# Kernel optimization log

Measured on AMD Instinct MI355X. Metric: run time of the kernel, lower is better.

## Reference

```python
import jax, jax.numpy as jnp
import numpy as np

B, T, VOCAB_SZ, N_SPK = 64, 1024, 34, 128
D_TXT, D_SPK, H, N_MELS = 512, 64, 256, 80


def _lstm_params(key, in_dim, hid):
    k1, k2, k3, k4 = jax.random.split(key, 4)
    s = 1.0 / np.sqrt(hid)
    Wih = jax.random.uniform(k1, (4 * hid, in_dim), jnp.float32, -s, s)
    Whh = jax.random.uniform(k2, (4 * hid, hid), jnp.float32, -s, s)
    bih = jax.random.uniform(k3, (4 * hid,), jnp.float32, -s, s)
    bhh = jax.random.uniform(k4, (4 * hid,), jnp.float32, -s, s)
    return Wih, Whh, bih, bhh


def setup_inputs() -> dict:
    key = jax.random.key(0)
    ks = jax.random.split(key, 10)
    text_seq = jax.random.randint(ks[0], (B, T), 0, VOCAB_SZ)
    mel_spectrogram = jax.random.normal(ks[1], (B, T, N_MELS), jnp.float32)
    speaker_id = jax.random.randint(ks[2], (B,), 0, N_SPK)
    emb_text = jax.random.normal(ks[3], (VOCAB_SZ, D_TXT), jnp.float32)
    emb_text = emb_text.at[0].set(0.0)  # padding_idx=0
    emb_spk = jax.random.normal(ks[4], (N_SPK, D_SPK), jnp.float32)
    Wih_f, Whh_f, bih_f, bhh_f = _lstm_params(ks[5], D_TXT + D_SPK, H)
    Wih_b, Whh_b, bih_b, bhh_b = _lstm_params(ks[6], D_TXT + D_SPK, H)
    Wih_d, _Whh_d, bih_d, bhh_d = _lstm_params(ks[7], N_MELS + 2 * H, H)
    s = 1.0 / np.sqrt(H)
    Wfc = jax.random.uniform(ks[8], (N_MELS, H), jnp.float32, -s, s)
    bfc = jax.random.uniform(ks[9], (N_MELS,), jnp.float32, -s, s)
    return dict(text_seq=text_seq, mel_spectrogram=mel_spectrogram, speaker_id=speaker_id,
                emb_text=emb_text, emb_spk=emb_spk,
                Wih_f=Wih_f, Whh_f=Whh_f, bih_f=bih_f, bhh_f=bhh_f,
                Wih_b=Wih_b, Whh_b=Whh_b, bih_b=bih_b, bhh_b=bhh_b,
                Wih_d=Wih_d, bih_d=bih_d, bhh_d=bhh_d, Wfc=Wfc, bfc=bfc)


def _lstm_scan(xs, Wih, Whh, bih, bhh, reverse=False):
    # xs: [T, B, D] -> hs: [T, B, H] (PyTorch gate order i,f,g,o)
    nB, hid = xs.shape[1], Whh.shape[1]
    bias = bih + bhh
    def step(carry, x):
        h, c = carry
        g = x @ Wih.T + h @ Whh.T + bias
        i, f, gg, o = jnp.split(g, 4, axis=-1)
        c = jax.nn.sigmoid(f) * c + jax.nn.sigmoid(i) * jnp.tanh(gg)
        h = jax.nn.sigmoid(o) * jnp.tanh(c)
        return (h, c), h
    init = (jnp.zeros((nB, hid), xs.dtype), jnp.zeros((nB, hid), xs.dtype))
    _, hs = jax.lax.scan(step, init, xs, reverse=reverse)
    return hs


def reference(text_seq, mel_spectrogram, speaker_id, emb_text, emb_spk,
              Wih_f, Whh_f, bih_f, bhh_f, Wih_b, Whh_b, bih_b, bhh_b,
              Wih_d, bih_d, bhh_d, Wfc, bfc):
    text_embed = emb_text[text_seq]                       # [B, T, 512]
    spk = jnp.broadcast_to(emb_spk[speaker_id][:, None, :],
                           (text_seq.shape[0], text_seq.shape[1], emb_spk.shape[1]))
    enc_in = jnp.concatenate([text_embed, spk], axis=-1)  # [B, T, 576]
    xs = jnp.transpose(enc_in, (1, 0, 2))                 # time-major [T, B, 576]
    h_fwd = _lstm_scan(xs, Wih_f, Whh_f, bih_f, bhh_f)
    h_bwd = _lstm_scan(xs, Wih_b, Whh_b, bih_b, bhh_b, reverse=True)
    enc_out = jnp.concatenate([h_fwd, h_bwd], axis=-1)    # [T, B, 512]

    max_len = min(mel_spectrogram.shape[1], enc_out.shape[0])
    # Decoder: hidden state is reset (None) every step in the original, so
    # c = sigmoid(i)*tanh(g), h = sigmoid(o)*tanh(c); Whh contributes nothing.
    dbias = bih_d + bhh_d
    def dstep(prev_mel, e_t):
        x = jnp.concatenate([prev_mel, e_t], axis=-1)     # [B, 592]
        g = x @ Wih_d.T + dbias
        i, f, gg, o = jnp.split(g, 4, axis=-1)
        c = jax.nn.sigmoid(i) * jnp.tanh(gg)
        h = jax.nn.sigmoid(o) * jnp.tanh(c)
        out = h @ Wfc.T + bfc
        return out, out
    _, outs = jax.lax.scan(dstep, mel_spectrogram[:, 0, :], enc_out[: max_len - 1])
    return jnp.transpose(outs, (1, 0, 2))                 # [B, max_len-1, 80]
```

## Files before the change

kernel.cpp:

```cpp
#include <hip/hip_runtime.h>
#include <hip/hip_fp16.h>
#include <stdint.h>

#define T_SEQ 1024
#define NB    64
#define VOCAB 34
#define NSPK  128
#define DTXT  512
#define HID   256
#define NMEL  80
#define GROWS 1024
#define DROWS 768

typedef _Float16 f16;
typedef _Float16 f16x2 __attribute__((ext_vector_type(2)));
typedef _Float16 v8h __attribute__((ext_vector_type(8)));
typedef float v4f __attribute__((ext_vector_type(4)));

__device__ __forceinline__ float fdot2f(uint32_t a, uint32_t b, float c) {
  return __builtin_amdgcn_fdot2(__builtin_bit_cast(f16x2, a),
                                __builtin_bit_cast(f16x2, b), c, false);
}
__device__ __forceinline__ float sigm(float x) { return 1.0f / (1.0f + __expf(-x)); }
__device__ __forceinline__ float tanhf_fast(float x) {
  float e = __expf(2.0f * x);
  return 1.0f - 2.0f / (e + 1.0f);
}
__device__ __forceinline__ void bar_vperm() {
  asm volatile("s_waitcnt lgkmcnt(0)\n\ts_barrier" ::: "memory");
  __builtin_amdgcn_sched_barrier(0);
}


__global__ void k_tp(const float* __restrict__ Wf, const float* __restrict__ Wb,
                     const float* __restrict__ emb_text, float* __restrict__ TP) {
  int blk = blockIdx.x; int dir = blk / VOCAB; int v = blk - dir * VOCAB;
  const float* W = dir ? Wb : Wf;
  const float4* e4 = (const float4*)(emb_text + (size_t)v * DTXT);
  for (int r = threadIdx.x; r < GROWS; r += 256) {
    const float4* w4 = (const float4*)(W + (size_t)r * 576);
    float a0 = 0, a1 = 0, a2 = 0, a3 = 0;
    #pragma unroll 4
    for (int d = 0; d < DTXT / 4; ++d) {
      float4 ev = e4[d], wv = w4[d];
      a0 += ev.x * wv.x; a1 += ev.y * wv.y;
      a2 += ev.z * wv.z; a3 += ev.w * wv.w;
    }
    TP[(size_t)(dir * VOCAB + v) * GROWS + r] = (a0 + a1) + (a2 + a3);
  }
}

__global__ void k_sp(const float* __restrict__ Wf, const float* __restrict__ Wb,
                     const float* __restrict__ bihf, const float* __restrict__ bhhf,
                     const float* __restrict__ bihb, const float* __restrict__ bhhb,
                     const float* __restrict__ emb_spk, float* __restrict__ SP) {
  int blk = blockIdx.x; int dir = blk >> 7; int s = blk & 127;
  const float* W  = dir ? Wb : Wf;
  const float* bi = dir ? bihb : bihf;
  const float* bh = dir ? bhhb : bhhf;
  const float4* e4 = (const float4*)(emb_spk + (size_t)s * 64);
  for (int r = threadIdx.x; r < GROWS; r += 256) {
    const float4* w4 = (const float4*)(W + (size_t)r * 576 + 512);
    float a0 = 0, a1 = 0, a2 = 0, a3 = 0;
    #pragma unroll
    for (int d = 0; d < 16; ++d) {
      float4 ev = e4[d], wv = w4[d];
      a0 += ev.x * wv.x; a1 += ev.y * wv.y;
      a2 += ev.z * wv.z; a3 += ev.w * wv.w;
    }
    SP[(size_t)(dir * NSPK + s) * GROWS + r] = bi[r] + bh[r] + (a0 + a1) + (a2 + a3);
  }
}

__global__ void k_whh(const float* __restrict__ Whhf, const float* __restrict__ Whhb,
                      f16* __restrict__ WhhH) {
  int idx = blockIdx.x * 256 + threadIdx.x;
  if (idx < 2 * GROWS * HID) {
    int dir = idx >> 18; int rem = idx & (GROWS * HID - 1);
    WhhH[idx] = (f16)(dir ? Whhb[rem] : Whhf[rem]);
  }
}

__global__ void k_decw(const float* __restrict__ Wih_d, const float* __restrict__ bih_d,
                       const float* __restrict__ bhh_d,
                       f16* __restrict__ WmH, f16* __restrict__ WdH, float* __restrict__ dbias) {
  int r = blockIdx.x;
  int src = (r < 256) ? r : (r + 256);
  const float* w = Wih_d + (size_t)src * 592;
  for (int k = threadIdx.x; k < 592; k += 256) {
    float v = w[k];
    if (k < 80) WmH[(size_t)r * 80 + k] = (f16)v;
    else        WdH[(size_t)r * 512 + (k - 80)] = (f16)v;
  }
  if (threadIdx.x == 0) dbias[r] = bih_d[src] + bhh_d[src];
}

__global__ void k_misc(const float* __restrict__ Wfc, f16* __restrict__ WfcH) {
  int idx = blockIdx.x * 256 + threadIdx.x;
  if (idx < NMEL * HID) WfcH[idx] = (f16)Wfc[idx];
}

__launch_bounds__(512, 2)
__global__ void k_enc(const int* __restrict__ text_seq, const int* __restrict__ speaker_id,
                      const float* __restrict__ TP, const float* __restrict__ SP,
                      const uint32_t* __restrict__ WhhH_dw,
                      f16* __restrict__ Hh) {
  __shared__ __align__(16) uint4 wtail[16 * 512];
  __shared__ __align__(16) uint32_t hbuf[2][128];
  __shared__ float pp[4][256];
  __shared__ int tseq[T_SEQ];

  int wg = blockIdx.x;
  int dir = wg >> 6, b = wg & 63;
  int tid = threadIdx.x;
  int u = tid & 255, kh = tid >> 8;

  uint4 w0[12], w1[12], w2[12], w3[12];
  {
    const uint4* p0 = (const uint4*)(WhhH_dw + ((size_t)(dir << 10) + u      ) * 128 + (kh << 6));
    const uint4* p1 = (const uint4*)(WhhH_dw + ((size_t)(dir << 10) + u + 256) * 128 + (kh << 6));
    const uint4* p2 = (const uint4*)(WhhH_dw + ((size_t)(dir << 10) + u + 512) * 128 + (kh << 6));
    const uint4* p3 = (const uint4*)(WhhH_dw + ((size_t)(dir << 10) + u + 768) * 128 + (kh << 6));
    #pragma unroll
    for (int i = 0; i < 12; ++i) { w0[i] = p0[i]; w1[i] = p1[i]; w2[i] = p2[i]; w3[i] = p3[i]; }
    #pragma unroll
    for (int j = 0; j < 4; ++j) {
      wtail[(0 * 4 + j) * 512 + tid] = p0[12 + j];
      wtail[(1 * 4 + j) * 512 + tid] = p1[12 + j];
      wtail[(2 * 4 + j) * 512 + tid] = p2[12 + j];
      wtail[(3 * 4 + j) * 512 + tid] = p3[12 + j];
    }
  }
  for (int i = tid; i < T_SEQ; i += 512) tseq[i] = text_seq[b * T_SEQ + i];
  if (tid < 128) hbuf[0][tid] = 0u;
  float sp0 = 0, sp1 = 0, sp2 = 0, sp3 = 0;
  if (kh == 0) {
    int spk = speaker_id[b];
    sp0 = SP[(size_t)(dir * NSPK + spk) * GROWS + u];
    sp1 = SP[(size_t)(dir * NSPK + spk) * GROWS + u + 256];
    sp2 = SP[(size_t)(dir * NSPK + spk) * GROWS + u + 512];
    sp3 = SP[(size_t)(dir * NSPK + spk) * GROWS + u + 768];
  }
  const float* TPd = TP + (size_t)dir * VOCAB * GROWS;
  float c_state = 0.0f;
  __syncthreads();

  float x0 = 0, x1 = 0, x2 = 0, x3 = 0;
  if (kh == 0) {
    int v = tseq[dir ? (T_SEQ - 1) : 0];
    x0 = TPd[(size_t)v * GROWS + u];
    x1 = TPd[(size_t)v * GROWS + u + 256];
    x2 = TPd[(size_t)v * GROWS + u + 512];
    x3 = TPd[(size_t)v * GROWS + u + 768];
  }

  float h_keep = 0.0f; int t_keep = 0;
  for (int n = 0; n < T_SEQ; ++n) {
    int t = dir ? (T_SEQ - 1 - n) : n;
    float xn0 = 0, xn1 = 0, xn2 = 0, xn3 = 0;
    if (kh == 0) {
      if (n > 0)
        Hh[((size_t)(dir * T_SEQ + t_keep) * NB + b) * HID + u] = (f16)h_keep;
      int tn = dir ? (T_SEQ - 2 - n) : (n + 1);
      tn = tn < 0 ? 0 : (tn > T_SEQ - 1 ? T_SEQ - 1 : tn);
      int vn = tseq[tn];
      xn0 = TPd[(size_t)vn * GROWS + u];
      xn1 = TPd[(size_t)vn * GROWS + u + 256];
      xn2 = TPd[(size_t)vn * GROWS + u + 512];
      xn3 = TPd[(size_t)vn * GROWS + u + 768];
    }

    float i0 = 0, i1 = 0, f0 = 0, f1 = 0, g0 = 0, g1 = 0, o0 = 0, o1 = 0;
    const uint4* h4 = ((const uint4*)hbuf[n & 1]) + (kh << 4);
    #pragma unroll
    for (int c = 0; c < 12; ++c) {
      uint4 hv = h4[c];
      i0 = fdot2f(w0[c].x, hv.x, i0); f0 = fdot2f(w1[c].x, hv.x, f0);
      g0 = fdot2f(w2[c].x, hv.x, g0); o0 = fdot2f(w3[c].x, hv.x, o0);
      i1 = fdot2f(w0[c].y, hv.y, i1); f1 = fdot2f(w1[c].y, hv.y, f1);
      g1 = fdot2f(w2[c].y, hv.y, g1); o1 = fdot2f(w3[c].y, hv.y, o1);
      i0 = fdot2f(w0[c].z, hv.z, i0); f0 = fdot2f(w1[c].z, hv.z, f0);
      g0 = fdot2f(w2[c].z, hv.z, g0); o0 = fdot2f(w3[c].z, hv.z, o0);
      i1 = fdot2f(w0[c].w, hv.w, i1); f1 = fdot2f(w1[c].w, hv.w, f1);
      g1 = fdot2f(w2[c].w, hv.w, g1); o1 = fdot2f(w3[c].w, hv.w, o1);
    }
    #pragma unroll
    for (int j = 0; j < 4; ++j) {
      uint4 hv = h4[12 + j];
      uint4 t0v = wtail[(0 * 4 + j) * 512 + tid];
      uint4 t1v = wtail[(1 * 4 + j) * 512 + tid];
      uint4 t2v = wtail[(2 * 4 + j) * 512 + tid];
      uint4 t3v = wtail[(3 * 4 + j) * 512 + tid];
      i0 = fdot2f(t0v.x, hv.x, i0); f0 = fdot2f(t1v.x, hv.x, f0);
      g0 = fdot2f(t2v.x, hv.x, g0); o0 = fdot2f(t3v.x, hv.x, o0);
      i1 = fdot2f(t0v.y, hv.y, i1); f1 = fdot2f(t1v.y, hv.y, f1);
      g1 = fdot2f(t2v.y, hv.y, g1); o1 = fdot2f(t3v.y, hv.y, o1);
      i0 = fdot2f(t0v.z, hv.z, i0); f0 = fdot2f(t1v.z, hv.z, f0);
      g0 = fdot2f(t2v.z, hv.z, g0); o0 = fdot2f(t3v.z, hv.z, o0);
      i1 = fdot2f(t0v.w, hv.w, i1); f1 = fdot2f(t1v.w, hv.w, f1);
      g1 = fdot2f(t2v.w, hv.w, g1); o1 = fdot2f(t3v.w, hv.w, o1);
    }
    if (kh == 1) {
      pp[0][u] = i0 + i1;
      pp[1][u] = f0 + f1;
      pp[2][u] = g0 + g1;
      pp[3][u] = o0 + o1;
    }
    bar_vperm();

    if (kh == 0) {
      float gi = (i0 + i1) + pp[0][u] + x0 + sp0;
      float gf = (f0 + f1) + pp[1][u] + x1 + sp1;
      float gg = (g0 + g1) + pp[2][u] + x2 + sp2;
      float go = (o0 + o1) + pp[3][u] + x3 + sp3;
      c_state = sigm(gf) * c_state + sigm(gi) * tanhf_fast(gg);
      float h = sigm(go) * tanhf_fast(c_state);
      ((f16*)hbuf[(n + 1) & 1])[u] = (f16)h;
      h_keep = h; t_keep = t;
      x0 = xn0; x1 = xn1; x2 = xn2; x3 = xn3;
    }
    bar_vperm();
  }
  if (kh == 0)
    Hh[((size_t)(dir * T_SEQ + t_keep) * NB + b) * HID + u] = (f16)h_keep;
}

__launch_bounds__(256, 4)
__global__ void k_eproj(const uint32_t* __restrict__ Hdw, const uint32_t* __restrict__ WdH_dw,
                        const float* __restrict__ dbias, f16* __restrict__ E) {
  __shared__ __align__(16) uint32_t Asm[64][68];
  __shared__ __align__(16) uint32_t Wsm[64][68];
  int nt = blockIdx.x % 12;
  int t  = blockIdx.x / 12;
  int n0 = nt * 64;
  int tid = threadIdx.x;
  int wave = tid >> 6, lane = tid & 63;
  int lr = lane & 15, lg = lane >> 4;

  v4f acc0 = {0,0,0,0}, acc1 = {0,0,0,0}, acc2 = {0,0,0,0}, acc3 = {0,0,0,0};

  for (int ch = 0; ch < 4; ++ch) {
    int dirc = ch >> 1, koff = (ch & 1) * 64;
    {
      int bb = tid >> 2, p = tid & 3;
      const uint32_t* asrc = Hdw + ((size_t)(dirc * T_SEQ + t) * NB + bb) * 128 + koff + p * 4;
      const uint32_t* wsrc = WdH_dw + (size_t)(n0 + bb) * 256 + ch * 64 + p * 4;
      #pragma unroll
      for (int q = 0; q < 4; ++q) {
        *(uint4*)(&Asm[bb][p * 4 + q * 16]) = *(const uint4*)(asrc + q * 16);
        *(uint4*)(&Wsm[bb][p * 4 + q * 16]) = *(const uint4*)(wsrc + q * 16);
      }
    }
    __syncthreads();
    #pragma unroll
    for (int sub = 0; sub < 4; ++sub) {
      v8h af = __builtin_bit_cast(v8h, *(const uint4*)&Asm[wave * 16 + lr][sub * 16 + lg * 4]);
      v8h b0 = __builtin_bit_cast(v8h, *(const uint4*)&Wsm[ 0 + lr][sub * 16 + lg * 4]);
      v8h b1 = __builtin_bit_cast(v8h, *(const uint4*)&Wsm[16 + lr][sub * 16 + lg * 4]);
      v8h b2 = __builtin_bit_cast(v8h, *(const uint4*)&Wsm[32 + lr][sub * 16 + lg * 4]);
      v8h b3 = __builtin_bit_cast(v8h, *(const uint4*)&Wsm[48 + lr][sub * 16 + lg * 4]);
      acc0 = __builtin_amdgcn_mfma_f32_16x16x32_f16(af, b0, acc0, 0, 0, 0);
      acc1 = __builtin_amdgcn_mfma_f32_16x16x32_f16(af, b1, acc1, 0, 0, 0);
      acc2 = __builtin_amdgcn_mfma_f32_16x16x32_f16(af, b2, acc2, 0, 0, 0);
      acc3 = __builtin_amdgcn_mfma_f32_16x16x32_f16(af, b3, acc3, 0, 0, 0);
    }
    __syncthreads();
  }

  float db0 = dbias[n0 +  0 + lr];
  float db1 = dbias[n0 + 16 + lr];
  float db2 = dbias[n0 + 32 + lr];
  float db3 = dbias[n0 + 48 + lr];
  #pragma unroll
  for (int reg = 0; reg < 4; ++reg) {
    int m = wave * 16 + lg * 4 + reg;
    f16* Erow = E + ((size_t)t * NB + m) * DROWS + n0;
    Erow[ 0 + lr] = (f16)(acc0[reg] + db0);
    Erow[16 + lr] = (f16)(acc1[reg] + db1);
    Erow[32 + lr] = (f16)(acc2[reg] + db2);
    Erow[48 + lr] = (f16)(acc3[reg] + db3);
  }
}

__launch_bounds__(512, 2)
__global__ void k_dec(const float* __restrict__ mel, const f16* __restrict__ E,
                      const uint32_t* __restrict__ WmH_dw, const uint32_t* __restrict__ WfcH_dw,
                      const float* __restrict__ bfc, float* __restrict__ out) {
  __shared__ __align__(16) uint32_t pm[40];
  __shared__ __align__(16) uint32_t h_sm[128];
  __shared__ float pp[3][256];
  __shared__ float partial[80][4];
  __shared__ __align__(16) uint4 Ebuf[2][16 * 96];

  int b = blockIdx.x;
  int tid = threadIdx.x;
  int u = tid & 255, kh = tid >> 8;

  uint4 wm0[5], wm1[5], wm2[5];
  {
    const uint4* p0 = (const uint4*)(WmH_dw + (size_t)(u      ) * 40) + kh * 5;
    const uint4* p1 = (const uint4*)(WmH_dw + (size_t)(u + 256) * 40) + kh * 5;
    const uint4* p2 = (const uint4*)(WmH_dw + (size_t)(u + 512) * 40) + kh * 5;
    #pragma unroll
    for (int k = 0; k < 5; ++k) { wm0[k] = p0[k]; wm1[k] = p1[k]; wm2[k] = p2[k]; }
  }
  int fr = (tid < 320) ? (tid >> 2) : 0;
  int q  = tid & 3;
  uint4 wfc[8];
  {
    const uint4* wp = (const uint4*)(WfcH_dw + (size_t)fr * 128) + q * 8;
    #pragma unroll
    for (int k = 0; k < 8; ++k) wfc[k] = wp[k];
  }
  float bfcv = bfc[tid < NMEL ? tid : 0];
  if (tid < 40) {
    float m0 = mel[(size_t)b * T_SEQ * NMEL + 2 * tid];
    float m1 = mel[(size_t)b * T_SEQ * NMEL + 2 * tid + 1];
    f16x2 v; v[0] = (f16)m0; v[1] = (f16)m1;
    pm[tid] = __builtin_bit_cast(uint32_t, v);
  }

  int srow = tid >> 5, scol = tid & 31;
  {
    const uint4* src = (const uint4*)(E + ((size_t)srow * NB + b) * DROWS);
    Ebuf[0][srow * 96 + scol     ] = src[scol];
    Ebuf[0][srow * 96 + scol + 32] = src[scol + 32];
    Ebuf[0][srow * 96 + scol + 64] = src[scol + 64];
  }
  __syncthreads();

  float o_keep = 0.0f;
  for (int t = 0; t < T_SEQ - 1; ++t) {
    int w = t >> 4, s = t & 15;
    if (t > 0 && tid < NMEL)
      out[((size_t)b * (T_SEQ - 1) + (t - 1)) * NMEL + tid] = o_keep;
    uint4 st0, st1, st2;
    bool do_stage = (s == 0) && (w < 63);
    if (do_stage) {
      int rr = (w + 1) * 16 + srow; if (rr > T_SEQ - 2) rr = T_SEQ - 2;
      const uint4* src = (const uint4*)(E + ((size_t)rr * NB + b) * DROWS);
      st0 = src[scol]; st1 = src[scol + 32]; st2 = src[scol + 64];
    }

    float a0 = 0, a1 = 0, a2 = 0;
    const uint4* pm4 = ((const uint4*)pm) + kh * 5;
    #pragma unroll
    for (int k = 0; k < 5; ++k) {
      uint4 hp = pm4[k];
      a0 = fdot2f(wm0[k].x, hp.x, a0); a1 = fdot2f(wm1[k].x, hp.x, a1); a2 = fdot2f(wm2[k].x, hp.x, a2);
      a0 = fdot2f(wm0[k].y, hp.y, a0); a1 = fdot2f(wm1[k].y, hp.y, a1); a2 = fdot2f(wm2[k].y, hp.y, a2);
      a0 = fdot2f(wm0[k].z, hp.z, a0); a1 = fdot2f(wm1[k].z, hp.z, a1); a2 = fdot2f(wm2[k].z, hp.z, a2);
      a0 = fdot2f(wm0[k].w, hp.w, a0); a1 = fdot2f(wm1[k].w, hp.w, a1); a2 = fdot2f(wm2[k].w, hp.w, a2);
    }
    if (kh == 1) { pp[0][u] = a0; pp[1][u] = a1; pp[2][u] = a2; }
    __syncthreads();

    if (kh == 0) {
      const f16* Erow = (const f16*)&Ebuf[w & 1][s * 96];
      float gi = a0 + pp[0][u] + (float)Erow[u];
      float gg = a1 + pp[1][u] + (float)Erow[u + 256];
      float go = a2 + pp[2][u] + (float)Erow[u + 512];
      float cc = sigm(gi) * tanhf_fast(gg);
      float h  = sigm(go) * tanhf_fast(cc);
      ((f16*)h_sm)[u] = (f16)h;
    }
    if (do_stage) {
      Ebuf[(w + 1) & 1][srow * 96 + scol     ] = st0;
      Ebuf[(w + 1) & 1][srow * 96 + scol + 32] = st1;
      Ebuf[(w + 1) & 1][srow * 96 + scol + 64] = st2;
    }
    __syncthreads();

    if (tid < 320) {
      const uint4* hrow = ((const uint4*)h_sm) + q * 8;
      float s0 = 0, s1 = 0, s2 = 0, s3 = 0;
      #pragma unroll
      for (int kk = 0; kk < 8; ++kk) {
        uint4 hq = hrow[kk];
        s0 = fdot2f(wfc[kk].x, hq.x, s0); s1 = fdot2f(wfc[kk].y, hq.y, s1);
        s2 = fdot2f(wfc[kk].z, hq.z, s2); s3 = fdot2f(wfc[kk].w, hq.w, s3);
      }
      partial[fr][q] = (s0 + s1) + (s2 + s3);
    }
    __syncthreads();

    if (tid < NMEL) {
      float o = ((partial[tid][0] + partial[tid][1]) +
                 (partial[tid][2] + partial[tid][3])) + bfcv;
      o_keep = o;
      ((f16*)pm)[tid] = (f16)o;
    }
    __syncthreads();
  }
  if (tid < NMEL)
    out[((size_t)b * (T_SEQ - 1) + (T_SEQ - 2)) * NMEL + tid] = o_keep;
}

extern "C" void kernel_launch(void* const* d_in, const int* in_sizes, int n_in,
                              void* d_out, int out_size, void* d_ws, size_t ws_size,
                              hipStream_t stream) {
  const int*   text_seq   = (const int*)d_in[0];
  const float* mel        = (const float*)d_in[1];
  const int*   speaker_id = (const int*)d_in[2];
  const float* emb_text   = (const float*)d_in[3];
  const float* emb_spk    = (const float*)d_in[4];
  const float* Wih_f = (const float*)d_in[5];
  const float* Whh_f = (const float*)d_in[6];
  const float* bih_f = (const float*)d_in[7];
  const float* bhh_f = (const float*)d_in[8];
  const float* Wih_b = (const float*)d_in[9];
  const float* Whh_b = (const float*)d_in[10];
  const float* bih_b = (const float*)d_in[11];
  const float* bhh_b = (const float*)d_in[12];
  const float* Wih_d = (const float*)d_in[13];
  const float* bih_d = (const float*)d_in[14];
  const float* bhh_d = (const float*)d_in[15];
  const float* Wfc   = (const float*)d_in[16];
  const float* bfc   = (const float*)d_in[17];
  float* out = (float*)d_out;

  char* base = (char*)d_ws;
  size_t off = 0;
  auto take = [&](size_t n) -> char* {
    off = (off + 255) & ~(size_t)255;
    char* r = base + off;
    off += n;
    return r;
  };
  float*        TP    = (float*)take((size_t)2 * VOCAB * GROWS * 4);
  float*        SP    = (float*)take((size_t)2 * NSPK * GROWS * 4);
  f16*          WhhH  = (f16*)take((size_t)2 * GROWS * HID * 2);
  f16*          WmH   = (f16*)take((size_t)DROWS * 80 * 2);
  f16*          WdH   = (f16*)take((size_t)DROWS * 512 * 2);
  f16*          WfcH  = (f16*)take((size_t)NMEL * HID * 2);
  float*        dbias = (float*)take((size_t)DROWS * 4);
  f16*          Hh    = (f16*)take((size_t)2 * T_SEQ * NB * HID * 2);
  f16*          E     = (f16*)take((size_t)(T_SEQ - 1) * NB * DROWS * 2);
  if (off > ws_size) return;

  k_tp  <<<2 * VOCAB, 256, 0, stream>>>(Wih_f, Wih_b, emb_text, TP);
  k_sp  <<<2 * NSPK, 256, 0, stream>>>(Wih_f, Wih_b, bih_f, bhh_f, bih_b, bhh_b, emb_spk, SP);
  k_whh <<<2048, 256, 0, stream>>>(Whh_f, Whh_b, WhhH);
  k_decw<<<DROWS, 256, 0, stream>>>(Wih_d, bih_d, bhh_d, WmH, WdH, dbias);
  k_misc<<<80, 256, 0, stream>>>(Wfc, WfcH);
  k_enc <<<128, 512, 0, stream>>>(text_seq, speaker_id, TP, SP,
                                  (const uint32_t*)WhhH, Hh);
  k_eproj<<<(T_SEQ - 1) * 12, 256, 0, stream>>>((const uint32_t*)Hh,
                                                (const uint32_t*)WdH, dbias, E);
  k_dec <<<NB, 512, 0, stream>>>(mel, E, (const uint32_t*)WmH,
                                 (const uint32_t*)WfcH, bfc, out);
}
```

Baseline: 2.834 ms.

## Split each encoder LSTM sequence across two workgroups with flag-based hidden-state exchange

The encoder recurrence now runs on two workgroups per (direction, batch) pair instead of one. Each workgroup owns half of the hidden units, keeps its full Whh rows in registers (dropping the LDS weight tail and the intra-block k-split reduction), and exchanges its half of h with its partner every step through global memory, using release/acquire flags that k_misc zeroes beforehand. This halves the per-step dot-product work and register/LDS pressure per workgroup and uses more CUs. In exchange it adds a cross-workgroup global-memory handshake on the serial critical path every timestep, and it deadlocks if the two partner workgroups are not co-resident. A large dummy LDS allocation is added, apparently to limit occupancy to one block per CU.

```diff
diff --git a/kernel.cpp b/kernel.cpp
--- a/kernel.cpp
+++ b/kernel.cpp
@@ -95,134 +95,102 @@
   if (threadIdx.x == 0) dbias[r] = bih_d[src] + bhh_d[src];
 }
 
-__global__ void k_misc(const float* __restrict__ Wfc, f16* __restrict__ WfcH) {
+__global__ void k_misc(const float* __restrict__ Wfc, f16* __restrict__ WfcH,
+                       unsigned int* __restrict__ flags) {
   int idx = blockIdx.x * 256 + threadIdx.x;
   if (idx < NMEL * HID) WfcH[idx] = (f16)Wfc[idx];
+  if (blockIdx.x == 0) flags[threadIdx.x * 64] = 0u;
 }
 
 __launch_bounds__(512, 2)
 __global__ void k_enc(const int* __restrict__ text_seq, const int* __restrict__ speaker_id,
                       const float* __restrict__ TP, const float* __restrict__ SP,
                       const uint32_t* __restrict__ WhhH_dw,
-                      f16* __restrict__ Hh) {
-  __shared__ __align__(16) uint4 wtail[16 * 512];
-  __shared__ __align__(16) uint32_t hbuf[2][128];
-  __shared__ float pp[4][256];
+                      f16* __restrict__ Hh, uint32_t* __restrict__ Hx,
+                      unsigned int* __restrict__ flags) {
+  __shared__ __align__(16) uint32_t hfull[2][128];
+  __shared__ float pp[512];
   __shared__ int tseq[T_SEQ];
-
-  int wg = blockIdx.x;
-  int dir = wg >> 6, b = wg & 63;
+  __shared__ __align__(16) uint4 lds_pad[4800];
+
+  int wgid = blockIdx.x;
+  int pair = wgid & 127, half = wgid >> 7;
+  int dir = pair >> 6, b = pair & 63;
   int tid = threadIdx.x;
-  int u = tid & 255, kh = tid >> 8;
-
-  uint4 w0[12], w1[12], w2[12], w3[12];
+  int g = tid >> 7, uu = tid & 127;
+  int row = g * 256 + half * 128 + uu;
+
+  uint4 w[32];
   {
-    const uint4* p0 = (const uint4*)(WhhH_dw + ((size_t)(dir << 10) + u      ) * 128 + (kh << 6));
-    const uint4* p1 = (const uint4*)(WhhH_dw + ((size_t)(dir << 10) + u + 256) * 128 + (kh << 6));
-    const uint4* p2 = (const uint4*)(WhhH_dw + ((size_t)(dir << 10) + u + 512) * 128 + (kh << 6));
-    const uint4* p3 = (const uint4*)(WhhH_dw + ((size_t)(dir << 10) + u + 768) * 128 + (kh << 6));
-    #pragma unroll
-    for (int i = 0; i < 12; ++i) { w0[i] = p0[i]; w1[i] = p1[i]; w2[i] = p2[i]; w3[i] = p3[i]; }
-    #pragma unroll
-    for (int j = 0; j < 4; ++j) {
-      wtail[(0 * 4 + j) * 512 + tid] = p0[12 + j];
-      wtail[(1 * 4 + j) * 512 + tid] = p1[12 + j];
-      wtail[(2 * 4 + j) * 512 + tid] = p2[12 + j];
-      wtail[(3 * 4 + j) * 512 + tid] = p3[12 + j];
-    }
+    const uint4* wp = (const uint4*)(WhhH_dw + ((size_t)(dir << 10) + row) * 128);
+    #pragma unroll
+    for (int i = 0; i < 32; ++i) w[i] = wp[i];
   }
   for (int i = tid; i < T_SEQ; i += 512) tseq[i] = text_seq[b * T_SEQ + i];
-  if (tid < 128) hbuf[0][tid] = 0u;
-  float sp0 = 0, sp1 = 0, sp2 = 0, sp3 = 0;
-  if (kh == 0) {
-    int spk = speaker_id[b];
-    sp0 = SP[(size_t)(dir * NSPK + spk) * GROWS + u];
-    sp1 = SP[(size_t)(dir * NSPK + spk) * GROWS + u + 256];
-    sp2 = SP[(size_t)(dir * NSPK + spk) * GROWS + u + 512];
-    sp3 = SP[(size_t)(dir * NSPK + spk) * GROWS + u + 768];
-  }
+  if (tid < 128) hfull[0][tid] = 0u;
+  ((volatile uint32_t*)lds_pad)[tid] = 0u;
+  float sp = SP[(size_t)(dir * NSPK + speaker_id[b]) * GROWS + row];
   const float* TPd = TP + (size_t)dir * VOCAB * GROWS;
   float c_state = 0.0f;
+  const unsigned myF = (unsigned)(pair * 2 + half);
+  const unsigned paF = (unsigned)(pair * 2 + (half ^ 1));
   __syncthreads();
 
-  float x0 = 0, x1 = 0, x2 = 0, x3 = 0;
-  if (kh == 0) {
-    int v = tseq[dir ? (T_SEQ - 1) : 0];
-    x0 = TPd[(size_t)v * GROWS + u];
-    x1 = TPd[(size_t)v * GROWS + u + 256];
-    x2 = TPd[(size_t)v * GROWS + u + 512];
-    x3 = TPd[(size_t)v * GROWS + u + 768];
-  }
-
-  float h_keep = 0.0f; int t_keep = 0;
+  float xcur = TPd[(size_t)tseq[dir ? (T_SEQ - 1) : 0] * GROWS + row];
+
   for (int n = 0; n < T_SEQ; ++n) {
     int t = dir ? (T_SEQ - 1 - n) : n;
-    float xn0 = 0, xn1 = 0, xn2 = 0, xn3 = 0;
-    if (kh == 0) {
-      if (n > 0)
-        Hh[((size_t)(dir * T_SEQ + t_keep) * NB + b) * HID + u] = (f16)h_keep;
-      int tn = dir ? (T_SEQ - 2 - n) : (n + 1);
-      tn = tn < 0 ? 0 : (tn > T_SEQ - 1 ? T_SEQ - 1 : tn);
-      int vn = tseq[tn];
-      xn0 = TPd[(size_t)vn * GROWS + u];
-      xn1 = TPd[(size_t)vn * GROWS + u + 256];
-      xn2 = TPd[(size_t)vn * GROWS + u + 512];
-      xn3 = TPd[(size_t)vn * GROWS + u + 768];
-    }
-
-    float i0 = 0, i1 = 0, f0 = 0, f1 = 0, g0 = 0, g1 = 0, o0 = 0, o1 = 0;
-    const uint4* h4 = ((const uint4*)hbuf[n & 1]) + (kh << 4);
-    #pragma unroll
-    for (int c = 0; c < 12; ++c) {
+    int tn = dir ? (T_SEQ - 2 - n) : (n + 1);
+    tn = tn < 0 ? 0 : (tn > T_SEQ - 1 ? T_SEQ - 1 : tn);
+    float xnext = TPd[(size_t)tseq[tn] * GROWS + row];
+
+    float a0 = 0, a1 = 0, a2 = 0, a3 = 0;
+    const uint4* h4 = (const uint4*)hfull[n & 1];
+    #pragma unroll
+    for (int c = 0; c < 32; ++c) {
       uint4 hv = h4[c];
-      i0 = fdot2f(w0[c].x, hv.x, i0); f0 = fdot2f(w1[c].x, hv.x, f0);
-      g0 = fdot2f(w2[c].x, hv.x, g0); o0 = fdot2f(w3[c].x, hv.x, o0);
-      i1 = fdot2f(w0[c].y, hv.y, i1); f1 = fdot2f(w1[c].y, hv.y, f1);
-      g1 = fdot2f(w2[c].y, hv.y, g1); o1 = fdot2f(w3[c].y, hv.y, o1);
-      i0 = fdot2f(w0[c].z, hv.z, i0); f0 = fdot2f(w1[c].z, hv.z, f0);
-      g0 = fdot2f(w2[c].z, hv.z, g0); o0 = fdot2f(w3[c].z, hv.z, o0);
-      i1 = fdot2f(w0[c].w, hv.w, i1); f1 = fdot2f(w1[c].w, hv.w, f1);
-      g1 = fdot2f(w2[c].w, hv.w, g1); o1 = fdot2f(w3[c].w, hv.w, o1);
-    }
-    #pragma unroll
-    for (int j = 0; j < 4; ++j) {
-      uint4 hv = h4[12 + j];
-      uint4 t0v = wtail[(0 * 4 + j) * 512 + tid];
-      uint4 t1v = wtail[(1 * 4 + j) * 512 + tid];
-      uint4 t2v = wtail[(2 * 4 + j) * 512 + tid];
-      uint4 t3v = wtail[(3 * 4 + j) * 512 + tid];
-      i0 = fdot2f(t0v.x, hv.x, i0); f0 = fdot2f(t1v.x, hv.x, f0);
-      g0 = fdot2f(t2v.x, hv.x, g0); o0 = fdot2f(t3v.x, hv.x, o0);
-      i1 = fdot2f(t0v.y, hv.y, i1); f1 = fdot2f(t1v.y, hv.y, f1);
-      g1 = fdot2f(t2v.y, hv.y, g1); o1 = fdot2f(t3v.y, hv.y, o1);
-      i0 = fdot2f(t0v.z, hv.z, i0); f0 = fdot2f(t1v.z, hv.z, f0);
-      g0 = fdot2f(t2v.z, hv.z, g0); o0 = fdot2f(t3v.z, hv.z, o0);
-      i1 = fdot2f(t0v.w, hv.w, i1); f1 = fdot2f(t1v.w, hv.w, f1);
-      g1 = fdot2f(t2v.w, hv.w, g1); o1 = fdot2f(t3v.w, hv.w, o1);
-    }
-    if (kh == 1) {
-      pp[0][u] = i0 + i1;
-      pp[1][u] = f0 + f1;
-      pp[2][u] = g0 + g1;
-      pp[3][u] = o0 + o1;
-    }
+      a0 = fdot2f(w[c].x, hv.x, a0);
+      a1 = fdot2f(w[c].y, hv.y, a1);
+      a2 = fdot2f(w[c].z, hv.z, a2);
+      a3 = fdot2f(w[c].w, hv.w, a3);
+    }
+    pp[tid] = ((a0 + a1) + (a2 + a3)) + xcur + sp;
     bar_vperm();
 
-    if (kh == 0) {
-      float gi = (i0 + i1) + pp[0][u] + x0 + sp0;
-      float gf = (f0 + f1) + pp[1][u] + x1 + sp1;
-      float gg = (g0 + g1) + pp[2][u] + x2 + sp2;
-      float go = (o0 + o1) + pp[3][u] + x3 + sp3;
+    if (tid < 128) {
+      float gi = pp[uu], gf = pp[128 + uu], gg = pp[256 + uu], go = pp[384 + uu];
       c_state = sigm(gf) * c_state + sigm(gi) * tanhf_fast(gg);
       float h = sigm(go) * tanhf_fast(c_state);
-      ((f16*)hbuf[(n + 1) & 1])[u] = (f16)h;
-      h_keep = h; t_keep = t;
-      x0 = xn0; x1 = xn1; x2 = xn2; x3 = xn3;
+      ((f16*)hfull[(n + 1) & 1])[half * 128 + uu] = (f16)h;
     }
     bar_vperm();
-  }
-  if (kh == 0)
-    Hh[((size_t)(dir * T_SEQ + t_keep) * NB + b) * HID + u] = (f16)h_keep;
+
+    if (n < T_SEQ - 1) {
+      if (tid < 16) {
+        uint4 d = *(const uint4*)&hfull[(n + 1) & 1][half * 64 + tid * 4];
+        *(uint4*)(Hx + ((size_t)(myF * 2u + (unsigned)((n + 1) & 1)) * 64) + tid * 4) = d;
+        if (tid == 0)
+          __hip_atomic_store(&flags[myF * 64], (unsigned)(n + 1),
+                             __ATOMIC_RELEASE, __HIP_MEMORY_SCOPE_AGENT);
+        *(uint4*)(Hh + ((size_t)(dir * T_SEQ + t) * NB + b) * HID + half * 128 + tid * 8) = d;
+      } else if (tid >= 64 && tid < 80) {
+        int lt = tid - 64;
+        const unsigned* pf = &flags[paF * 64];
+        while (__hip_atomic_load(pf, __ATOMIC_RELAXED, __HIP_MEMORY_SCOPE_AGENT)
+               < (unsigned)(n + 1)) {}
+        (void)__hip_atomic_load(pf, __ATOMIC_ACQUIRE, __HIP_MEMORY_SCOPE_AGENT);
+        uint4 d = *(const uint4*)(Hx + ((size_t)(paF * 2u + (unsigned)((n + 1) & 1)) * 64) + lt * 4);
+        *(uint4*)&hfull[(n + 1) & 1][(half ^ 1) * 64 + lt * 4] = d;
+      }
+    } else {
+      if (tid < 16) {
+        uint4 d = *(const uint4*)&hfull[(n + 1) & 1][half * 64 + tid * 4];
+        *(uint4*)(Hh + ((size_t)(dir * T_SEQ + t) * NB + b) * HID + half * 128 + tid * 8) = d;
+      }
+    }
+    xcur = xnext;
+    bar_vperm();
+  }
 }
 
 __launch_bounds__(256, 4)
@@ -434,6 +402,8 @@
   f16*          WdH   = (f16*)take((size_t)DROWS * 512 * 2);
   f16*          WfcH  = (f16*)take((size_t)NMEL * HID * 2);
   float*        dbias = (float*)take((size_t)DROWS * 4);
+  unsigned int* flags = (unsigned int*)take((size_t)256 * 64 * 4);
+  uint32_t*     Hx    = (uint32_t*)take((size_t)256 * 2 * 64 * 4);
   f16*          Hh    = (f16*)take((size_t)2 * T_SEQ * NB * HID * 2);
   f16*          E     = (f16*)take((size_t)(T_SEQ - 1) * NB * DROWS * 2);
   if (off > ws_size) return;
@@ -442,9 +412,9 @@
   k_sp  <<<2 * NSPK, 256, 0, stream>>>(Wih_f, Wih_b, bih_f, bhh_f, bih_b, bhh_b, emb_spk, SP);
   k_whh <<<2048, 256, 0, stream>>>(Whh_f, Whh_b, WhhH);
   k_decw<<<DROWS, 256, 0, stream>>>(Wih_d, bih_d, bhh_d, WmH, WdH, dbias);
-  k_misc<<<80, 256, 0, stream>>>(Wfc, WfcH);
-  k_enc <<<128, 512, 0, stream>>>(text_seq, speaker_id, TP, SP,
-                                  (const uint32_t*)WhhH, Hh);
+  k_misc<<<80, 256, 0, stream>>>(Wfc, WfcH, flags);
+  k_enc <<<256, 512, 0, stream>>>(text_seq, speaker_id, TP, SP,
+                                  (const uint32_t*)WhhH, Hh, Hx, flags);
   k_eproj<<<(T_SEQ - 1) * 12, 256, 0, stream>>>((const uint32_t*)Hh,
                                                 (const uint32_t*)WdH, dbias, E);
   k_dec <<<NB, 512, 0, stream>>>(mel, E, (const uint32_t*)WmH,
```

Result: slower. 6.139 ms (+116.6%).
